# Kernel tuning notes

Measured on AMD Instinct MI355X. Metric: run time of the kernel, lower is better.

Reference implementation:

```python
import jax, jax.numpy as jnp
import numpy as np

N = 50000   # nodes
E = 500000  # edges
S = 64      # 0e channels in node feats
V = 32      # 1o channels in node feats
R = 32      # radial/scalar edge features
MLPW = 128
AVG = 10.0  # avg_num_neighbors
SQ3 = np.float32(np.sqrt(3.0))
SQ2 = np.float32(np.sqrt(2.0))


def setup_inputs() -> dict:
    key = jax.random.key(0)
    ks = jax.random.split(key, 10)
    node_scalars = jax.random.normal(ks[0], (N, S), jnp.float32)
    node_vectors = jax.random.normal(ks[1], (N, V, 3), jnp.float32)
    ev = jax.random.normal(ks[2], (E, 3), jnp.float32)
    # l=1 spherical harmonics of unit edge vectors, component normalization (|Y1| = sqrt(3))
    edge_vec = ev / jnp.linalg.norm(ev, axis=1, keepdims=True) * SQ3
    scalar_edge_feats = jax.random.normal(ks[3], (E, R), jnp.float32)
    lengths = jax.random.uniform(ks[4], (E, 1), jnp.float32)
    senders = jax.random.randint(ks[5], (E,), 0, N, jnp.int32)
    receivers = jax.random.randint(ks[6], (E,), 0, N, jnp.int32)
    din = 2 * S + R + 1  # 161
    num_irreps = V + (S + V)  # 128 gate scalars
    def lin(k, i, o):
        return jax.random.normal(k, (i, o), jnp.float32) / np.float32(np.sqrt(i))
    return {
        "node_scalars": node_scalars, "node_vectors": node_vectors,
        "edge_vec": edge_vec, "scalar_edge_feats": scalar_edge_feats,
        "lengths": lengths, "senders": senders, "receivers": receivers,
        "W1": lin(ks[7], din, MLPW), "b1": jnp.zeros((MLPW,), jnp.float32),
        "W2": lin(ks[8], MLPW, MLPW), "b2": jnp.zeros((MLPW,), jnp.float32),
        "W3": lin(ks[9], MLPW, num_irreps), "b3": jnp.zeros((num_irreps,), jnp.float32),
    }


def reference(node_scalars, node_vectors, edge_vec, scalar_edge_feats, lengths,
              senders, receivers, W1, b1, W2, b2, W3, b3):
    # gather sender features
    s_snd = node_scalars[senders]          # [E, S]
    v_snd = node_vectors[senders]          # [E, V, 3]
    # Clebsch-Gordan tensor product with 1o edge harmonics (component normalization):
    m0 = jnp.einsum('eca,ea->ec', v_snd, edge_vec) / SQ3          # 1o x 1o -> 0e, [E, V]
    m1a = s_snd[:, :, None] * edge_vec[:, None, :]                 # 0e x 1o -> 1o, [E, S, 3]
    m1b = jnp.cross(v_snd, edge_vec[:, None, :]) / SQ2             # 1o x 1o -> 1o, [E, V, 3]
    # MLP gate on concatenated scalars
    mlp_in = jnp.concatenate([s_snd, node_scalars[receivers], scalar_edge_feats, lengths], axis=1)
    h = jax.nn.silu(mlp_in @ W1 + b1)
    h = jax.nn.silu(h @ W2 + b2)
    mix = h @ W3 + b3                                               # [E, V + S + V]
    m0 = m0 * mix[:, :V]
    m1 = jnp.concatenate([m1a, m1b], axis=1) * mix[:, V:, None]     # [E, S+V, 3]
    # scatter-add to receivers
    out0 = jax.ops.segment_sum(m0, receivers, num_segments=N)      # [N, V]
    out1 = jax.ops.segment_sum(m1, receivers, num_segments=N)      # [N, S+V, 3]
    return jnp.concatenate([out0, out1.reshape(N, -1)], axis=1) / AVG
```

## Files before the change

kernel.cpp:

```cpp
#include <hip/hip_runtime.h>

#define N_NODES 50000
#define N_EDGES 500000
#define EB 64
#define AST 184
#define HST 136
#define W1K 176
#define OUTC 320
#define NBLK1 49
#define KP1 200
#define KH  136
#define KV  104
#define WTS 40
#define INV_SQ3 0.57735026918962576f
#define INV_SQ2 0.70710678118654752f
#define INV_AVG 0.1f

typedef short bf16x8 __attribute__((ext_vector_type(8)));
typedef unsigned short u16;
typedef u16 u16x8 __attribute__((ext_vector_type(8)));
typedef float f32x16 __attribute__((ext_vector_type(16)));

template <int N> struct IC { static constexpr int val = N; };

__device__ __forceinline__ unsigned cvtpk(float lo, float hi) {
    unsigned r;
    asm("v_cvt_pk_bf16_f32 %0, %1, %2" : "=v"(r) : "v"(lo), "v"(hi));
    return r;
}
__device__ __forceinline__ u16 f2bf(float f) { return (u16)cvtpk(f, f); }
__device__ __forceinline__ float bf2f(u16 h) {
    union { unsigned u; float f; } x; x.u = ((unsigned)h) << 16; return x.f;
}
__device__ __forceinline__ float fsilu(float x) {
    return x * __builtin_amdgcn_rcpf(1.f + __expf(-x));
}

__device__ __forceinline__ void stage16(const float* g, u16* l, bool v) {
    float4 a0, a1, a2, a3;
    const float4 z = make_float4(0.f, 0.f, 0.f, 0.f);
    if (v) { a0 = *(const float4*)(g);     a1 = *(const float4*)(g + 4);
             a2 = *(const float4*)(g + 8); a3 = *(const float4*)(g + 12); }
    else   { a0 = z; a1 = z; a2 = z; a3 = z; }
    uint4 p0 = { cvtpk(a0.x, a0.y), cvtpk(a0.z, a0.w), cvtpk(a1.x, a1.y), cvtpk(a1.z, a1.w) };
    uint4 p1 = { cvtpk(a2.x, a2.y), cvtpk(a2.z, a2.w), cvtpk(a3.x, a3.y), cvtpk(a3.z, a3.w) };
    *(uint4*)(l) = p0; *(uint4*)(l + 8) = p1;
}
__device__ __forceinline__ void stage8(const float* g, u16* l, bool v) {
    float4 a0, a1;
    const float4 z = make_float4(0.f, 0.f, 0.f, 0.f);
    if (v) { a0 = *(const float4*)(g); a1 = *(const float4*)(g + 4); }
    else   { a0 = z; a1 = z; }
    uint4 p0 = { cvtpk(a0.x, a0.y), cvtpk(a0.z, a0.w), cvtpk(a1.x, a1.y), cvtpk(a1.z, a1.w) };
    *(uint4*)(l) = p0;
}


__global__ void hist_kernel(const int* __restrict__ recv, int* __restrict__ counts) {
    const int e = blockIdx.x * 256 + threadIdx.x;
    if (e < N_EDGES) atomicAdd(&counts[recv[e]], 1);
}

__global__ __launch_bounds__(256) void scan_k1(const int* __restrict__ counts,
                                               int* __restrict__ rowp,
                                               int* __restrict__ partials) {
    __shared__ int sd[256];
    const int t = threadIdx.x;
    const int base = blockIdx.x * 1024 + t * 4;
    int c0 = 0, c1 = 0, c2 = 0, c3 = 0;
    if (base + 3 < N_NODES) {
        int4 v = *(const int4*)&counts[base];
        c0 = v.x; c1 = v.y; c2 = v.z; c3 = v.w;
    } else {
        if (base     < N_NODES) c0 = counts[base];
        if (base + 1 < N_NODES) c1 = counts[base + 1];
        if (base + 2 < N_NODES) c2 = counts[base + 2];
        if (base + 3 < N_NODES) c3 = counts[base + 3];
    }
    const int T = c0 + c1 + c2 + c3;
    sd[t] = T; __syncthreads();
    for (int off = 1; off < 256; off <<= 1) {
        int v = (t >= off) ? sd[t - off] : 0;
        __syncthreads();
        sd[t] += v;
        __syncthreads();
    }
    const int excl = sd[t] - T;
    if (base     < N_NODES) rowp[base]     = excl;
    if (base + 1 < N_NODES) rowp[base + 1] = excl + c0;
    if (base + 2 < N_NODES) rowp[base + 2] = excl + c0 + c1;
    if (base + 3 < N_NODES) rowp[base + 3] = excl + c0 + c1 + c2;
    if (t == 255) partials[blockIdx.x] = sd[255];
}

__global__ __launch_bounds__(64) void scan_k2(int* __restrict__ partials) {
    __shared__ int sd[64];
    const int t = threadIdx.x;
    const int v0 = (t < NBLK1) ? partials[t] : 0;
    sd[t] = v0; __syncthreads();
    for (int off = 1; off < 64; off <<= 1) {
        int v = (t >= off) ? sd[t - off] : 0;
        __syncthreads();
        sd[t] += v;
        __syncthreads();
    }
    if (t < NBLK1) partials[t] = sd[t] - v0;
}

__global__ __launch_bounds__(256) void scan_k3(int* __restrict__ rowp,
                                               const int* __restrict__ partials,
                                               int* __restrict__ cursors) {
    const int add = partials[blockIdx.x];
    const int base = blockIdx.x * 1024 + threadIdx.x * 4;
    #pragma unroll
    for (int i = 0; i < 4; ++i) {
        const int idx = base + i;
        if (idx < N_NODES) {
            const int v = rowp[idx] + add;
            rowp[idx] = v;
            cursors[idx] = v;
        }
    }
    if (blockIdx.x == 0 && threadIdx.x == 0) rowp[N_NODES] = N_EDGES;
}

__global__ void fill_kernel(const int* __restrict__ recv,
                            int* __restrict__ cursors, int* __restrict__ elist) {
    const int e = blockIdx.x * 256 + threadIdx.x;
    if (e < N_EDGES) {
        const int r = recv[e];
        const int pos = atomicAdd(&cursors[r], 1);
        elist[pos] = e;
    }
}


#define WT_TOTAL (128 * W1K + 2 * 128 * 128)

__global__ __launch_bounds__(256)
void wcvt_kernel(const float* __restrict__ W1, const float* __restrict__ W2,
                 const float* __restrict__ W3, u16* __restrict__ wt) {
    const int i = blockIdx.x * 256 + threadIdx.x;
    if (i < 128 * W1K) {
        const int n = i / W1K, k = i - n * W1K;
        wt[i] = (k < 161) ? f2bf(W1[(size_t)k * 128 + n]) : (u16)0;
    } else if (i < 128 * W1K + 128 * 128) {
        const int j = i - 128 * W1K;
        const int n = j >> 7, k = j & 127;
        wt[i] = f2bf(W2[(size_t)k * 128 + n]);
    } else if (i < WT_TOTAL) {
        const int j = i - 128 * W1K - 128 * 128;
        const int n = j >> 7, k = j & 127;
        wt[i] = f2bf(W3[(size_t)k * 128 + n]);
    }
}


#define NS_ELEMS (N_NODES * 64)
#define NV_ELEMS (N_NODES * 96)

__global__ __launch_bounds__(256)
void nodecvt_kernel(const float* __restrict__ ns, const float* __restrict__ nv,
                    u16* __restrict__ nsb, u16* __restrict__ nvb) {
    const int i2 = (blockIdx.x * 256 + threadIdx.x) * 2;
    if (i2 < NS_ELEMS) {
        float2 v = *(const float2*)(ns + i2);
        *(unsigned*)(nsb + i2) = cvtpk(v.x, v.y);
    } else if (i2 < NS_ELEMS + NV_ELEMS) {
        const int j2 = i2 - NS_ELEMS;
        float2 v = *(const float2*)(nv + j2);
        *(unsigned*)(nvb + j2) = cvtpk(v.x, v.y);
    }
}


__global__ __launch_bounds__(256, 4)
void mlp_msg_kernel(const u16* __restrict__ ns_bf,
                    const u16* __restrict__ nv_bf,
                    const float* __restrict__ edge_vec,
                    const float* __restrict__ sef,
                    const float* __restrict__ lengths,
                    const int* __restrict__ senders,
                    const int* __restrict__ receivers,
                    const int* __restrict__ elist,
                    const u16* __restrict__ wt,
                    const float* __restrict__ b1,
                    const float* __restrict__ b2,
                    const float* __restrict__ b3,
                    u16* __restrict__ msg, int slo, int cnt)
{
    __shared__ u16 A [EB * AST];
    __shared__ u16 Hb[EB * HST];

    const int t = threadIdx.x;
    const int lbase = blockIdx.x * EB;
    const int me = t >> 2, q = t & 3;
    const int ls = lbase + me;
    const bool ve = ls < cnt;
    const int eid = ve ? elist[slo + ls] : 0;

    {   const int si = senders[eid];
        const int ri = receivers[eid];
        u16* Ar = A + me * AST;
        const u16* srow = ns_bf + (size_t)si * 64 + q * 16;
        const u16* rrow = ns_bf + (size_t)ri * 64 + q * 16;
        *(u16x8*)(Ar + q * 16)          = *(const u16x8*)(srow);
        *(u16x8*)(Ar + q * 16 + 8)      = *(const u16x8*)(srow + 8);
        *(u16x8*)(Ar + 64 + q * 16)     = *(const u16x8*)(rrow);
        *(u16x8*)(Ar + 64 + q * 16 + 8) = *(const u16x8*)(rrow + 8);
        stage8(sef + (size_t)eid * 32 + q * 8, Ar + 128 + q * 8, true);
        if (q == 0) {
            u16x8 z8 = (u16x8)0;
            z8[0] = f2bf(lengths[eid]);
            *(u16x8*)(Ar + 160) = z8;
            const float evx = edge_vec[(size_t)eid * 3 + 0];
            const float evy = edge_vec[(size_t)eid * 3 + 1];
            const float evz = edge_vec[(size_t)eid * 3 + 2];
            const unsigned bx = __builtin_bit_cast(unsigned, evx);
            const unsigned by = __builtin_bit_cast(unsigned, evy);
            const unsigned bz = __builtin_bit_cast(unsigned, evz);
            u16x8 p;
            p[0] = (u16)(bx & 0xFFFF); p[1] = (u16)(bx >> 16);
            p[2] = (u16)(by & 0xFFFF); p[3] = (u16)(by >> 16);
            p[4] = (u16)(bz & 0xFFFF); p[5] = (u16)(bz >> 16);
            p[6] = (u16)si;            p[7] = 0;
            *(u16x8*)(Hb + me * HST + 128) = p;
        } else if (q == 1) {
            *(u16x8*)(A + me * AST + 168) = (u16x8)0;
        }
    }
    __syncthreads();

    const int w  = t >> 6, l = t & 63;
    const int lr = l & 31;
    const int lg = l >> 5;
    const int m0 = (w >> 1) * 32;
    const int n0 = (w & 1) * 64;

    const u16* w1t = wt;
    const u16* w2t = wt + 128 * W1K;
    const u16* w3t = w2t + 128 * 128;

    f32x16 acc0, acc1;

    auto run_layer = [&](const u16* Asrc, int astr, const u16* Wg, int wstr, auto NS,
                         f32x16& a0, f32x16& a1) {
        #pragma unroll
        for (int i = 0; i < 16; ++i) { a0[i] = 0.f; a1[i] = 0.f; }
        const u16* ap  = Asrc + (m0 + lr) * astr + lg * 8;
        const u16* bp0 = Wg + (size_t)(n0 + lr) * wstr + lg * 8;
        const u16* bp1 = bp0 + 32 * wstr;
        #pragma unroll
        for (int ks = 0; ks < NS.val; ++ks) {
            bf16x8 af  = *(const bf16x8*)(ap  + ks * 16);
            bf16x8 bv0 = *(const bf16x8*)(bp0 + ks * 16);
            bf16x8 bv1 = *(const bf16x8*)(bp1 + ks * 16);
            a0 = __builtin_amdgcn_mfma_f32_32x32x16_bf16(af, bv0, a0, 0, 0, 0);
            a1 = __builtin_amdgcn_mfma_f32_32x32x16_bf16(af, bv1, a1, 0, 0, 0);
        }
    };

    run_layer(A, AST, w1t, W1K, IC<11>{}, acc0, acc1);
    __syncthreads();
    {   const float bv0 = b1[n0 + lr], bv1 = b1[n0 + 32 + lr];
        #pragma unroll
        for (int r = 0; r < 16; ++r) {
            const int row = (r & 3) + 8 * (r >> 2) + 4 * lg;
            Hb[(m0 + row) * HST + n0 + lr]      = f2bf(fsilu(acc0[r] + bv0));
            Hb[(m0 + row) * HST + n0 + 32 + lr] = f2bf(fsilu(acc1[r] + bv1));
        }
    }
    {
        const int si2 = (int)Hb[me * HST + 134];
        const u16* src = nv_bf + (size_t)si2 * 96 + q * 24;
        u16* dst = A + me * AST + 64 + q * 24;
        *(u16x8*)(dst)      = *(const u16x8*)(src);
        *(u16x8*)(dst + 8)  = *(const u16x8*)(src + 8);
        *(u16x8*)(dst + 16) = *(const u16x8*)(src + 16);
    }
    __syncthreads();

    run_layer(Hb, HST, w2t, 128, IC<8>{}, acc0, acc1);
    __syncthreads();
    {   const float bv0 = b2[n0 + lr], bv1 = b2[n0 + 32 + lr];
        #pragma unroll
        for (int r = 0; r < 16; ++r) {
            const int row = (r & 3) + 8 * (r >> 2) + 4 * lg;
            Hb[(m0 + row) * HST + n0 + lr]      = f2bf(fsilu(acc0[r] + bv0));
            Hb[(m0 + row) * HST + n0 + 32 + lr] = f2bf(fsilu(acc1[r] + bv1));
        }
    }
    __syncthreads();

    run_layer(Hb, HST, w3t, 128, IC<8>{}, acc0, acc1);
    __syncthreads();
    {   const float bv0 = b3[n0 + lr], bv1 = b3[n0 + 32 + lr];
        #pragma unroll
        for (int r = 0; r < 16; ++r) {
            const int row = (r & 3) + 8 * (r >> 2) + 4 * lg;
            Hb[(m0 + row) * HST + n0 + lr]      = f2bf(acc0[r] + bv0);
            Hb[(m0 + row) * HST + n0 + 32 + lr] = f2bf(acc1[r] + bv1);
        }
    }
    __syncthreads();

    if (ve) {
        const u16* Ar = A  + me * AST;
        const u16* Vr = Ar + 64;
        const u16* Hr = Hb + me * HST;
        const u16* Er = Hr + 128;
        u16* mrow = msg + (size_t)ls * 320;
        const float evx = __builtin_bit_cast(float, (unsigned)Er[0] | ((unsigned)Er[1] << 16));
        const float evy = __builtin_bit_cast(float, (unsigned)Er[2] | ((unsigned)Er[3] << 16));
        const float evz = __builtin_bit_cast(float, (unsigned)Er[4] | ((unsigned)Er[5] << 16));

        {
            float f[8];
            #pragma unroll
            for (int j = 0; j < 8; ++j) {
                const int c = 8 * q + j;
                const float vx = bf2f(Vr[3 * c]), vy = bf2f(Vr[3 * c + 1]), vz = bf2f(Vr[3 * c + 2]);
                f[j] = (vx * evx + vy * evy + vz * evz) * INV_SQ3 * bf2f(Hr[c]);
            }
            uint4 o = { cvtpk(f[0], f[1]), cvtpk(f[2], f[3]), cvtpk(f[4], f[5]), cvtpk(f[6], f[7]) };
            *(uint4*)(mrow + 8 * q) = o;
        }
        #pragma unroll
        for (int gg = 0; gg < 3; ++gg) {
            float fb[24];
            #pragma unroll
            for (int g8 = 0; g8 < 8; ++g8) {
                const int k = 24 * q + gg * 8 + g8;
                const float gate = bf2f(Hr[32 + k]);
                if (k < 64) {
                    const float s = bf2f(Ar[k]) * gate;
                    fb[3 * g8 + 0] = s * evx;
                    fb[3 * g8 + 1] = s * evy;
                    fb[3 * g8 + 2] = s * evz;
                } else {
                    const int c = k - 64;
                    const float vx = bf2f(Vr[3 * c]), vy = bf2f(Vr[3 * c + 1]), vz = bf2f(Vr[3 * c + 2]);
                    const float sc = INV_SQ2 * gate;
                    fb[3 * g8 + 0] = (vy * evz - vz * evy) * sc;
                    fb[3 * g8 + 1] = (vz * evx - vx * evz) * sc;
                    fb[3 * g8 + 2] = (vx * evy - vy * evx) * sc;
                }
            }
            u16* dst = mrow + 32 + 72 * q + 24 * gg;
            uint4 o0 = { cvtpk(fb[0],  fb[1]),  cvtpk(fb[2],  fb[3]),  cvtpk(fb[4],  fb[5]),  cvtpk(fb[6],  fb[7])  };
            uint4 o1 = { cvtpk(fb[8],  fb[9]),  cvtpk(fb[10], fb[11]), cvtpk(fb[12], fb[13]), cvtpk(fb[14], fb[15]) };
            uint4 o2 = { cvtpk(fb[16], fb[17]), cvtpk(fb[18], fb[19]), cvtpk(fb[20], fb[21]), cvtpk(fb[22], fb[23]) };
            *(uint4*)(dst)      = o0;
            *(uint4*)(dst + 8)  = o1;
            *(uint4*)(dst + 16) = o2;
        }
    }
}


__global__ __launch_bounds__(256)
void msg_gather_seq(const int* __restrict__ rowp,
                    const u16* __restrict__ msg,
                    float* __restrict__ out,
                    int slo, int shi, int first)
{
    const int gw = (blockIdx.x * 256 + threadIdx.x) >> 6;
    const int l  = threadIdx.x & 63;
    if (gw >= N_NODES || l >= 40) return;

    const int rp0 = rowp[gw], rp1 = rowp[gw + 1];
    const int lo = rp0 > slo ? rp0 : slo;
    const int hi = rp1 < shi ? rp1 : shi;
    const int n  = hi - lo;

    float acc[8] = {0.f, 0.f, 0.f, 0.f, 0.f, 0.f, 0.f, 0.f};
    const u16* mb = msg + (size_t)(lo - slo) * 320 + l * 8;

    int j = 0;
    for (; j + 3 < n; j += 4) {
        const u16x8 v0 = *(const u16x8*)(mb + (size_t)(j)     * 320);
        const u16x8 v1 = *(const u16x8*)(mb + (size_t)(j + 1) * 320);
        const u16x8 v2 = *(const u16x8*)(mb + (size_t)(j + 2) * 320);
        const u16x8 v3 = *(const u16x8*)(mb + (size_t)(j + 3) * 320);
        #pragma unroll
        for (int qq = 0; qq < 8; ++qq)
            acc[qq] += (bf2f(v0[qq]) + bf2f(v1[qq])) + (bf2f(v2[qq]) + bf2f(v3[qq]));
    }
    for (; j < n; ++j) {
        const u16x8 v0 = *(const u16x8*)(mb + (size_t)j * 320);
        #pragma unroll
        for (int qq = 0; qq < 8; ++qq) acc[qq] += bf2f(v0[qq]);
    }

    float* orow = out + (size_t)gw * OUTC + l * 8;
    if (first) {
        *(float4*)(orow)     = make_float4(acc[0] * INV_AVG, acc[1] * INV_AVG,
                                           acc[2] * INV_AVG, acc[3] * INV_AVG);
        *(float4*)(orow + 4) = make_float4(acc[4] * INV_AVG, acc[5] * INV_AVG,
                                           acc[6] * INV_AVG, acc[7] * INV_AVG);
    } else if (n > 0) {
        float4 p0 = *(const float4*)(orow);
        float4 p1 = *(const float4*)(orow + 4);
        p0.x += acc[0] * INV_AVG; p0.y += acc[1] * INV_AVG;
        p0.z += acc[2] * INV_AVG; p0.w += acc[3] * INV_AVG;
        p1.x += acc[4] * INV_AVG; p1.y += acc[5] * INV_AVG;
        p1.z += acc[6] * INV_AVG; p1.w += acc[7] * INV_AVG;
        *(float4*)(orow)     = p0;
        *(float4*)(orow + 4) = p1;
    }
}


__global__ __launch_bounds__(256, 2)
void fused_mpconv_atomic(const float* __restrict__ node_scalars,
                         const float* __restrict__ node_vectors,
                         const float* __restrict__ edge_vec,
                         const float* __restrict__ sef,
                         const float* __restrict__ lengths,
                         const int* __restrict__ senders,
                         const int* __restrict__ receivers,
                         const float* __restrict__ W1, const float* __restrict__ b1,
                         const float* __restrict__ W2, const float* __restrict__ b2,
                         const float* __restrict__ W3, const float* __restrict__ b3,
                         float* __restrict__ out)
{
    __shared__ u16 A [EB * KP1];
    __shared__ u16 VS[EB * KV];
    __shared__ u16 Hb[EB * KH];
    __shared__ u16 Wt[2][128 * WTS];
    __shared__ float evl[3][EB];
    __shared__ int sidx[EB], ridx[EB];

    const int t = threadIdx.x;
    const int ebase = blockIdx.x * EB;

    {   const int e = t & 63, sub = t >> 6;
        const int eg = ebase + e; const bool ve = eg < N_EDGES;
        if (sub == 0)      sidx[e] = ve ? senders[eg] : 0;
        else if (sub == 1) ridx[e] = ve ? receivers[eg] : 0;
        else if (sub == 2) {
            evl[0][e] = ve ? edge_vec[(size_t)eg * 3 + 0] : 0.f;
            evl[1][e] = ve ? edge_vec[(size_t)eg * 3 + 1] : 0.f;
            evl[2][e] = ve ? edge_vec[(size_t)eg * 3 + 2] : 0.f;
        }
    }
    __syncthreads();

    {   const int me = t >> 2, q = t & 3;
        const int eg = ebase + me; const bool ve = eg < N_EDGES;
        const int si = sidx[me], ri = ridx[me];
        u16* Ar = A + me * KP1;
        stage16(node_scalars + (size_t)si * 64 + q * 16, Ar + q * 16,       ve);
        stage16(node_scalars + (size_t)ri * 64 + q * 16, Ar + 64 + q * 16,  ve);
        stage8 (sef          + (size_t)eg * 32 + q * 8,  Ar + 128 + q * 8,  ve);
        u16x8 zz = (u16x8)0;
        *(u16x8*)(Ar + 160 + q * 8) = zz;
        if (q == 0) *(u16x8*)(Ar + 192) = zz;
        stage16(node_vectors + (size_t)si * 96 + q * 24,      VS + me * KV + q * 24,      ve);
        stage8 (node_vectors + (size_t)si * 96 + q * 24 + 16, VS + me * KV + q * 24 + 16, ve);
        if (q == 0) Ar[160] = f2bf(ve ? lengths[eg] : 0.f);
    }
    __syncthreads();

    const int w  = t >> 6, l = t & 63;
    const int lr = l & 31;
    const int lg = l >> 5;
    const int m0 = (w >> 1) * 32;
    const int n0 = (w & 1) * 64;

    f32x16 acc0, acc1;
    const int n  = t & 127, ph = t >> 7;

    auto run_layer = [&](const u16* Asrc, int astr, const float* Wg, int Kr, int nsteps,
                         f32x16& a0, f32x16& a1) {
        #pragma unroll
        for (int i = 0; i < 16; ++i) { a0[i] = 0.f; a1[i] = 0.f; }
        #pragma unroll
        for (int i = 0; i < 4; ++i) {
            int kl = (i * 2 + ph) * 2;
            float v0 = (kl     < Kr) ? Wg[(size_t)kl * 128 + n]       : 0.f;
            float v1 = (kl + 1 < Kr) ? Wg[(size_t)(kl + 1) * 128 + n] : 0.f;
            *(unsigned*)&Wt[0][n * WTS + kl] = cvtpk(v0, v1);
        }
        __syncthreads();
        const u16* ap = Asrc + (m0 + lr) * astr + lg * 8;
        for (int ks = 0; ks < nsteps; ++ks) {
            const int cur = ks & 1;
            float v0[4], v1[4];
            const int kb = (ks + 1) * 16;
            if (ks + 1 < nsteps) {
                #pragma unroll
                for (int i = 0; i < 4; ++i) {
                    int kg = kb + (i * 2 + ph) * 2;
                    v0[i] = (kg     < Kr) ? Wg[(size_t)kg * 128 + n]       : 0.f;
                    v1[i] = (kg + 1 < Kr) ? Wg[(size_t)(kg + 1) * 128 + n] : 0.f;
                }
            }
            bf16x8 af = *(const bf16x8*)(ap + ks * 16);
            bf16x8 bf0 = *(const bf16x8*)(&Wt[cur][(n0      + lr) * WTS + lg * 8]);
            bf16x8 bf1 = *(const bf16x8*)(&Wt[cur][(n0 + 32 + lr) * WTS + lg * 8]);
            a0 = __builtin_amdgcn_mfma_f32_32x32x16_bf16(af, bf0, a0, 0, 0, 0);
            a1 = __builtin_amdgcn_mfma_f32_32x32x16_bf16(af, bf1, a1, 0, 0, 0);
            if (ks + 1 < nsteps) {
                #pragma unroll
                for (int i = 0; i < 4; ++i) {
                    int kl = (i * 2 + ph) * 2;
                    *(unsigned*)&Wt[cur ^ 1][n * WTS + kl] = cvtpk(v0[i], v1[i]);
                }
            }
            __syncthreads();
        }
    };

    run_layer(A, KP1, W1, 161, 11, acc0, acc1);
    {   const float bv0 = b1[n0 + lr], bv1 = b1[n0 + 32 + lr];
        #pragma unroll
        for (int r = 0; r < 16; ++r) {
            const int row = (r & 3) + 8 * (r >> 2) + 4 * lg;
            Hb[(m0 + row) * KH + n0 + lr]      = f2bf(fsilu(acc0[r] + bv0));
            Hb[(m0 + row) * KH + n0 + 32 + lr] = f2bf(fsilu(acc1[r] + bv1));
        }
    }
    __syncthreads();

    run_layer(Hb, KH, W2, 128, 8, acc0, acc1);
    __syncthreads();
    {   const float bv0 = b2[n0 + lr], bv1 = b2[n0 + 32 + lr];
        #pragma unroll
        for (int r = 0; r < 16; ++r) {
            const int row = (r & 3) + 8 * (r >> 2) + 4 * lg;
            Hb[(m0 + row) * KH + n0 + lr]      = f2bf(fsilu(acc0[r] + bv0));
            Hb[(m0 + row) * KH + n0 + 32 + lr] = f2bf(fsilu(acc1[r] + bv1));
        }
    }
    __syncthreads();

    run_layer(Hb, KH, W3, 128, 8, acc0, acc1);
    __syncthreads();
    {   const float bv0 = b3[n0 + lr], bv1 = b3[n0 + 32 + lr];
        #pragma unroll
        for (int r = 0; r < 16; ++r) {
            const int row = (r & 3) + 8 * (r >> 2) + 4 * lg;
            Hb[(m0 + row) * KH + n0 + lr]      = f2bf(acc0[r] + bv0);
            Hb[(m0 + row) * KH + n0 + 32 + lr] = f2bf(acc1[r] + bv1);
        }
    }
    __syncthreads();

    {   const int me = t >> 2, r = t & 3;
        const int eg2 = ebase + me;
        if (eg2 < N_EDGES) {
            const int row = ridx[me];
            const float evx = evl[0][me], evy = evl[1][me], evz = evl[2][me];
            float* orow = out + (size_t)row * OUTC;
            const u16* Ar = A  + me * KP1;
            const u16* Vr = VS + me * KV;
            const u16* Hr = Hb + me * KH;
            for (int col = r; col < OUTC; col += 4) {
                float val;
                if (col < 32) {
                    const int c = col;
                    const float vx = bf2f(Vr[3 * c]), vy = bf2f(Vr[3 * c + 1]), vz = bf2f(Vr[3 * c + 2]);
                    val = (vx * evx + vy * evy + vz * evz) * INV_SQ3 * bf2f(Hr[c]);
                } else {
                    const int idx = col - 32;
                    const int k = idx / 3;
                    const int d = idx - 3 * k;
                    const float g = bf2f(Hr[32 + k]);
                    if (k < 64) {
                        const float evd = (d == 0) ? evx : ((d == 1) ? evy : evz);
                        val = bf2f(Ar[k]) * evd * g;
                    } else {
                        const int c = k - 64;
                        const float vx = bf2f(Vr[3 * c]), vy = bf2f(Vr[3 * c + 1]), vz = bf2f(Vr[3 * c + 2]);
                        float cr;
                        if (d == 0)      cr = vy * evz - vz * evy;
                        else if (d == 1) cr = vz * evx - vx * evz;
                        else             cr = vx * evy - vy * evx;
                        val = cr * INV_SQ2 * g;
                    }
                }
                atomicAdd(&orow[col], val * INV_AVG);
            }
        }
    }
}


extern "C" void kernel_launch(void* const* d_in, const int* in_sizes, int n_in,
                              void* d_out, int out_size, void* d_ws, size_t ws_size,
                              hipStream_t stream) {
    (void)in_sizes; (void)n_in;
    const float* node_scalars = (const float*)d_in[0];
    const float* node_vectors = (const float*)d_in[1];
    const float* edge_vec     = (const float*)d_in[2];
    const float* sef          = (const float*)d_in[3];
    const float* lengths      = (const float*)d_in[4];
    const int*   senders      = (const int*)d_in[5];
    const int*   receivers    = (const int*)d_in[6];
    const float* W1 = (const float*)d_in[7];
    const float* b1 = (const float*)d_in[8];
    const float* W2 = (const float*)d_in[9];
    const float* b2 = (const float*)d_in[10];
    const float* W3 = (const float*)d_in[11];
    const float* b3 = (const float*)d_in[12];
    float* out = (float*)d_out;

    auto align256 = [](size_t x) { return (x + 255) & ~(size_t)255; };

    size_t off = 0;
    const size_t o_counts  = off; off += align256((size_t)N_NODES * sizeof(int));
    const size_t o_rowp    = off; off += align256((size_t)(N_NODES + 1) * sizeof(int));
    const size_t o_cursors = off; off += align256((size_t)(N_NODES + 1) * sizeof(int));
    const size_t o_part    = off; off += align256(64 * sizeof(int));
    const size_t o_elist   = off; off += align256((size_t)N_EDGES * sizeof(int));
    const size_t o_wt      = off; off += align256((size_t)WT_TOTAL * sizeof(u16));
    const size_t o_nsb     = off; off += align256((size_t)NS_ELEMS * sizeof(u16));
    const size_t o_nvb     = off; off += align256((size_t)NV_ELEMS * sizeof(u16));
    const size_t o_msg     = off;
    const size_t fixed_bytes = off;

    long Ec = 0;
    if (ws_size > fixed_bytes + (size_t)128 * 640) {
        size_t cap_rows = (ws_size - fixed_bytes) / 640;
        Ec = ((long)cap_rows - 64) / 64 * 64;
        if (Ec > N_EDGES) Ec = N_EDGES;
    }

    char* ws = (char*)d_ws;

    if (Ec >= 64) {
        int* counts  = (int*)(ws + o_counts);
        int* rowp    = (int*)(ws + o_rowp);
        int* cursors = (int*)(ws + o_cursors);
        int* part    = (int*)(ws + o_part);
        int* elist   = (int*)(ws + o_elist);
        u16* wt      = (u16*)(ws + o_wt);
        u16* nsb     = (u16*)(ws + o_nsb);
        u16* nvb     = (u16*)(ws + o_nvb);
        u16* msg     = (u16*)(ws + o_msg);

        hipMemsetAsync(counts, 0, (size_t)N_NODES * sizeof(int), stream);
        hist_kernel<<<(N_EDGES + 255) / 256, 256, 0, stream>>>(receivers, counts);
        scan_k1<<<NBLK1, 256, 0, stream>>>(counts, rowp, part);
        scan_k2<<<1, 64, 0, stream>>>(part);
        scan_k3<<<NBLK1, 256, 0, stream>>>(rowp, part, cursors);
        fill_kernel<<<(N_EDGES + 255) / 256, 256, 0, stream>>>(receivers, cursors, elist);
        wcvt_kernel<<<(WT_TOTAL + 255) / 256, 256, 0, stream>>>(W1, W2, W3, wt);
        nodecvt_kernel<<<((NS_ELEMS + NV_ELEMS) / 2 + 255) / 256, 256, 0, stream>>>(
            node_scalars, node_vectors, nsb, nvb);

        const int nchunks = (int)((N_EDGES + Ec - 1) / Ec);
        const int ggrid = (N_NODES * 64 + 255) / 256;
        for (int c = 0; c < nchunks; ++c) {
            const int slo = (int)(c * Ec);
            const int cnt = (int)((N_EDGES - slo < Ec) ? (N_EDGES - slo) : Ec);
            mlp_msg_kernel<<<(cnt + EB - 1) / EB, 256, 0, stream>>>(
                nsb, nvb, edge_vec, sef, lengths, senders, receivers,
                elist, wt, b1, b2, b3, msg, slo, cnt);
            msg_gather_seq<<<ggrid, 256, 0, stream>>>(
                rowp, msg, out, slo, slo + cnt, c == 0 ? 1 : 0);
        }
    } else {
        hipMemsetAsync(out, 0, (size_t)out_size * sizeof(float), stream);
        fused_mpconv_atomic<<<(N_EDGES + EB - 1) / EB, 256, 0, stream>>>(
            node_scalars, node_vectors, edge_vec, sef, lengths,
            senders, receivers, W1, b1, W2, b2, W3, b3, out);
    }
}
```

Measured before the change: 444.3 us.

## Compress per-edge messages by deferring edge-vector outer product to the gather

Each edge message now stores the gated scalar values (64), m0 (32), the cross-product terms (96) and the raw edge vector in fp32, rather than the full 64x3 outer product. This shrinks each row from 320 to 208 bf16 values. The gather kernel rebuilds the m1a terms by multiplying each stored scalar by the edge vector while accumulating. It splits each node's edges across two half-waves and combines their partial sums through shared memory. The aim is to cut message write and read bandwidth, at the cost of extra FMAs, lane divergence by segment, and two block barriers in the gather.

```diff
diff --git a/kernel.cpp b/kernel.cpp
--- a/kernel.cpp
+++ b/kernel.cpp
@@ -7,6 +7,7 @@
 #define HST 136
 #define W1K 176
 #define OUTC 320
+#define MROW 208
 #define NBLK1 49
 #define KP1 200
 #define KH  136
@@ -309,50 +310,58 @@
         const u16* Vr = Ar + 64;
         const u16* Hr = Hb + me * HST;
         const u16* Er = Hr + 128;
-        u16* mrow = msg + (size_t)ls * 320;
+        u16* mrow = msg + (size_t)ls * MROW;
         const float evx = __builtin_bit_cast(float, (unsigned)Er[0] | ((unsigned)Er[1] << 16));
         const float evy = __builtin_bit_cast(float, (unsigned)Er[2] | ((unsigned)Er[3] << 16));
         const float evz = __builtin_bit_cast(float, (unsigned)Er[4] | ((unsigned)Er[5] << 16));
 
-        {
-            float f[8];
-            #pragma unroll
-            for (int j = 0; j < 8; ++j) {
-                const int c = 8 * q + j;
-                const float vx = bf2f(Vr[3 * c]), vy = bf2f(Vr[3 * c + 1]), vz = bf2f(Vr[3 * c + 2]);
-                f[j] = (vx * evx + vy * evy + vz * evz) * INV_SQ3 * bf2f(Hr[c]);
-            }
-            uint4 o = { cvtpk(f[0], f[1]), cvtpk(f[2], f[3]), cvtpk(f[4], f[5]), cvtpk(f[6], f[7]) };
+        float m0v[8], m1bv[24];
+        #pragma unroll
+        for (int j = 0; j < 8; ++j) {
+            const int c = 8 * q + j;
+            const float vx = bf2f(Vr[3 * c]), vy = bf2f(Vr[3 * c + 1]), vz = bf2f(Vr[3 * c + 2]);
+            m0v[j] = (vx * evx + vy * evy + vz * evz) * INV_SQ3 * bf2f(Hr[c]);
+            const float gb = bf2f(Hr[96 + c]) * INV_SQ2;
+            m1bv[3 * j + 0] = (vy * evz - vz * evy) * gb;
+            m1bv[3 * j + 1] = (vz * evx - vx * evz) * gb;
+            m1bv[3 * j + 2] = (vx * evy - vy * evx) * gb;
+        }
+        {   uint4 o = { cvtpk(m0v[0], m0v[1]), cvtpk(m0v[2], m0v[3]),
+                        cvtpk(m0v[4], m0v[5]), cvtpk(m0v[6], m0v[7]) };
             *(uint4*)(mrow + 8 * q) = o;
         }
-        #pragma unroll
-        for (int gg = 0; gg < 3; ++gg) {
-            float fb[24];
-            #pragma unroll
-            for (int g8 = 0; g8 < 8; ++g8) {
-                const int k = 24 * q + gg * 8 + g8;
-                const float gate = bf2f(Hr[32 + k]);
-                if (k < 64) {
-                    const float s = bf2f(Ar[k]) * gate;
-                    fb[3 * g8 + 0] = s * evx;
-                    fb[3 * g8 + 1] = s * evy;
-                    fb[3 * g8 + 2] = s * evz;
-                } else {
-                    const int c = k - 64;
-                    const float vx = bf2f(Vr[3 * c]), vy = bf2f(Vr[3 * c + 1]), vz = bf2f(Vr[3 * c + 2]);
-                    const float sc = INV_SQ2 * gate;
-                    fb[3 * g8 + 0] = (vy * evz - vz * evy) * sc;
-                    fb[3 * g8 + 1] = (vz * evx - vx * evz) * sc;
-                    fb[3 * g8 + 2] = (vx * evy - vy * evx) * sc;
-                }
-            }
-            u16* dst = mrow + 32 + 72 * q + 24 * gg;
-            uint4 o0 = { cvtpk(fb[0],  fb[1]),  cvtpk(fb[2],  fb[3]),  cvtpk(fb[4],  fb[5]),  cvtpk(fb[6],  fb[7])  };
-            uint4 o1 = { cvtpk(fb[8],  fb[9]),  cvtpk(fb[10], fb[11]), cvtpk(fb[12], fb[13]), cvtpk(fb[14], fb[15]) };
-            uint4 o2 = { cvtpk(fb[16], fb[17]), cvtpk(fb[18], fb[19]), cvtpk(fb[20], fb[21]), cvtpk(fb[22], fb[23]) };
+        {   u16* dst = mrow + 96 + 24 * q;
+            uint4 o0 = { cvtpk(m1bv[0],  m1bv[1]),  cvtpk(m1bv[2],  m1bv[3]),
+                         cvtpk(m1bv[4],  m1bv[5]),  cvtpk(m1bv[6],  m1bv[7])  };
+            uint4 o1 = { cvtpk(m1bv[8],  m1bv[9]),  cvtpk(m1bv[10], m1bv[11]),
+                         cvtpk(m1bv[12], m1bv[13]), cvtpk(m1bv[14], m1bv[15]) };
+            uint4 o2 = { cvtpk(m1bv[16], m1bv[17]), cvtpk(m1bv[18], m1bv[19]),
+                         cvtpk(m1bv[20], m1bv[21]), cvtpk(m1bv[22], m1bv[23]) };
             *(uint4*)(dst)      = o0;
             *(uint4*)(dst + 8)  = o1;
             *(uint4*)(dst + 16) = o2;
+        }
+        {   float sg[16];
+            #pragma unroll
+            for (int j = 0; j < 16; ++j) {
+                const int k = 16 * q + j;
+                sg[j] = bf2f(Ar[k]) * bf2f(Hr[32 + k]);
+            }
+            u16* dst = mrow + 32 + 16 * q;
+            uint4 o0 = { cvtpk(sg[0],  sg[1]),  cvtpk(sg[2],  sg[3]),
+                         cvtpk(sg[4],  sg[5]),  cvtpk(sg[6],  sg[7])  };
+            uint4 o1 = { cvtpk(sg[8],  sg[9]),  cvtpk(sg[10], sg[11]),
+                         cvtpk(sg[12], sg[13]), cvtpk(sg[14], sg[15]) };
+            *(uint4*)(dst)     = o0;
+            *(uint4*)(dst + 8) = o1;
+        }
+        if (q == 0) {
+            uint4 e4 = { __builtin_bit_cast(unsigned, evx),
+                         __builtin_bit_cast(unsigned, evy),
+                         __builtin_bit_cast(unsigned, evz), 0u };
+            *(uint4*)(mrow + 192) = e4;
+            uint4 z4 = { 0u, 0u, 0u, 0u };
+            *(uint4*)(mrow + 200) = z4;
         }
     }
 }
@@ -364,49 +373,110 @@
                     float* __restrict__ out,
                     int slo, int shi, int first)
 {
+    __shared__ float oacc[4][OUTC];
+
     const int gw = (blockIdx.x * 256 + threadIdx.x) >> 6;
     const int l  = threadIdx.x & 63;
-    if (gw >= N_NODES || l >= 40) return;
-
-    const int rp0 = rowp[gw], rp1 = rowp[gw + 1];
+    const bool nvalid = gw < N_NODES;
+
+    const int rp0 = nvalid ? rowp[gw] : 0;
+    const int rp1 = nvalid ? rowp[gw + 1] : 0;
     const int lo = rp0 > slo ? rp0 : slo;
     const int hi = rp1 < shi ? rp1 : shi;
-    const int n  = hi - lo;
-
-    float acc[8] = {0.f, 0.f, 0.f, 0.f, 0.f, 0.f, 0.f, 0.f};
-    const u16* mb = msg + (size_t)(lo - slo) * 320 + l * 8;
+    const int n  = hi > lo ? hi - lo : 0;
+
+    const int half = (l >= 26) ? 1 : 0;
+    const int sl   = l - 26 * half;
+    const bool lact = (l < 52) && (sl < 24);
+    const int seg  = (sl < 4) ? 0 : (sl < 12 ? 1 : 2);
+
+    float acc[24];
+    #pragma unroll
+    for (int i = 0; i < 24; ++i) acc[i] = 0.f;
+
+    const u16* mb = msg + (size_t)(lo - slo) * MROW;
+
+    auto body = [&](int row) {
+        const u16* rp = mb + (size_t)row * MROW + sl * 8;
+        const u16x8 v = *(const u16x8*)rp;
+        if (seg == 1) {
+            const float4 e4 = *(const float4*)(mb + (size_t)row * MROW + 192);
+            #pragma unroll
+            for (int i = 0; i < 8; ++i) {
+                const float s = bf2f(v[i]);
+                acc[3 * i + 0] += s * e4.x;
+                acc[3 * i + 1] += s * e4.y;
+                acc[3 * i + 2] += s * e4.z;
+            }
+        } else {
+            #pragma unroll
+            for (int i = 0; i < 8; ++i) acc[i] += bf2f(v[i]);
+        }
+    };
 
     int j = 0;
-    for (; j + 3 < n; j += 4) {
-        const u16x8 v0 = *(const u16x8*)(mb + (size_t)(j)     * 320);
-        const u16x8 v1 = *(const u16x8*)(mb + (size_t)(j + 1) * 320);
-        const u16x8 v2 = *(const u16x8*)(mb + (size_t)(j + 2) * 320);
-        const u16x8 v3 = *(const u16x8*)(mb + (size_t)(j + 3) * 320);
-        #pragma unroll
-        for (int qq = 0; qq < 8; ++qq)
-            acc[qq] += (bf2f(v0[qq]) + bf2f(v1[qq])) + (bf2f(v2[qq]) + bf2f(v3[qq]));
-    }
-    for (; j < n; ++j) {
-        const u16x8 v0 = *(const u16x8*)(mb + (size_t)j * 320);
-        #pragma unroll
-        for (int qq = 0; qq < 8; ++qq) acc[qq] += bf2f(v0[qq]);
-    }
-
-    float* orow = out + (size_t)gw * OUTC + l * 8;
-    if (first) {
-        *(float4*)(orow)     = make_float4(acc[0] * INV_AVG, acc[1] * INV_AVG,
-                                           acc[2] * INV_AVG, acc[3] * INV_AVG);
-        *(float4*)(orow + 4) = make_float4(acc[4] * INV_AVG, acc[5] * INV_AVG,
-                                           acc[6] * INV_AVG, acc[7] * INV_AVG);
-    } else if (n > 0) {
-        float4 p0 = *(const float4*)(orow);
-        float4 p1 = *(const float4*)(orow + 4);
-        p0.x += acc[0] * INV_AVG; p0.y += acc[1] * INV_AVG;
-        p0.z += acc[2] * INV_AVG; p0.w += acc[3] * INV_AVG;
-        p1.x += acc[4] * INV_AVG; p1.y += acc[5] * INV_AVG;
-        p1.z += acc[6] * INV_AVG; p1.w += acc[7] * INV_AVG;
-        *(float4*)(orow)     = p0;
-        *(float4*)(orow + 4) = p1;
+    for (; j + 2 <= n; j += 2) {
+        if (lact) body(j + half);
+    }
+    if (j < n && half == 0 && lact) body(j);
+
+    float* oa = oacc[(threadIdx.x >> 6)];
+
+    if (half == 0 && lact) {
+        if (seg == 0) {
+            #pragma unroll
+            for (int i = 0; i < 8; ++i) oa[sl * 8 + i] = acc[i];
+        } else if (seg == 1) {
+            const int k0 = (sl - 4) * 8;
+            #pragma unroll
+            for (int i = 0; i < 8; ++i) {
+                oa[32 + 3 * (k0 + i) + 0] = acc[3 * i + 0];
+                oa[32 + 3 * (k0 + i) + 1] = acc[3 * i + 1];
+                oa[32 + 3 * (k0 + i) + 2] = acc[3 * i + 2];
+            }
+        } else {
+            const int c0 = (sl - 12) * 8;
+            #pragma unroll
+            for (int i = 0; i < 8; ++i) oa[224 + c0 + i] = acc[i];
+        }
+    }
+    __syncthreads();
+    if (half == 1 && lact) {
+        if (seg == 0) {
+            #pragma unroll
+            for (int i = 0; i < 8; ++i) oa[sl * 8 + i] += acc[i];
+        } else if (seg == 1) {
+            const int k0 = (sl - 4) * 8;
+            #pragma unroll
+            for (int i = 0; i < 8; ++i) {
+                oa[32 + 3 * (k0 + i) + 0] += acc[3 * i + 0];
+                oa[32 + 3 * (k0 + i) + 1] += acc[3 * i + 1];
+                oa[32 + 3 * (k0 + i) + 2] += acc[3 * i + 2];
+            }
+        } else {
+            const int c0 = (sl - 12) * 8;
+            #pragma unroll
+            for (int i = 0; i < 8; ++i) oa[224 + c0 + i] += acc[i];
+        }
+    }
+    __syncthreads();
+
+    if (nvalid && l < 40) {
+        float r[8];
+        #pragma unroll
+        for (int i = 0; i < 8; ++i) r[i] = oa[l * 8 + i] * INV_AVG;
+        float* orow = out + (size_t)gw * OUTC + l * 8;
+        if (first) {
+            *(float4*)(orow)     = make_float4(r[0], r[1], r[2], r[3]);
+            *(float4*)(orow + 4) = make_float4(r[4], r[5], r[6], r[7]);
+        } else if (n > 0) {
+            float4 p0 = *(const float4*)(orow);
+            float4 p1 = *(const float4*)(orow + 4);
+            p0.x += r[0]; p0.y += r[1]; p0.z += r[2]; p0.w += r[3];
+            p1.x += r[4]; p1.y += r[5]; p1.z += r[6]; p1.w += r[7];
+            *(float4*)(orow)     = p0;
+            *(float4*)(orow + 4) = p1;
+        }
     }
 }
 
@@ -620,9 +690,10 @@
     const size_t o_msg     = off;
     const size_t fixed_bytes = off;
 
+    const size_t ROWB = (size_t)MROW * sizeof(u16);
     long Ec = 0;
-    if (ws_size > fixed_bytes + (size_t)128 * 640) {
-        size_t cap_rows = (ws_size - fixed_bytes) / 640;
+    if (ws_size > fixed_bytes + (size_t)128 * ROWB) {
+        size_t cap_rows = (ws_size - fixed_bytes) / ROWB;
         Ec = ((long)cap_rows - 64) / 64 * 64;
         if (Ec > N_EDGES) Ec = N_EDGES;
     }
```

Result: faster. 375.6 us (-15.5%).
